# Optimization experiments

Hardware: AMD Instinct MI355X
Metric: run time of the kernel (lower is better)

## Reference

```python
import jax, jax.numpy as jnp
import numpy as np

B, C, H, W, NH = 8, 256, 32, 32, 4  # batch, channels, height, width, heads


def groupnorm(x, w, b, eps=1e-5):
    # GroupNorm with 1 group: normalize over (C,H,W) per sample
    mu = x.mean(axis=(1, 2, 3), keepdims=True)
    var = x.var(axis=(1, 2, 3), keepdims=True)
    xn = (x - mu) * jax.lax.rsqrt(var + eps)
    return xn * w[None, :, None, None] + b[None, :, None, None]


def setup_inputs() -> dict:
    key = jax.random.key(0)
    ks = jax.random.split(key, 6)
    C4 = 4 * C
    s = lambda k, shape, scale: jax.random.normal(k, shape, jnp.float32) * scale
    return {
        "x": jax.random.normal(ks[0], (B, C, H, W), jnp.float32),
        "qkv_w": s(ks[1], (3 * C, C), 0.05),   # 1x1 conv, no bias
        "uh_w": s(ks[2], (C, C), 0.05),
        "uh_b": jnp.zeros((C,), jnp.float32),
        "n1_w": jnp.ones((C,), jnp.float32),
        "n1_b": jnp.zeros((C,), jnp.float32),
        "n2_w": jnp.ones((C,), jnp.float32),
        "n2_b": jnp.zeros((C,), jnp.float32),
        "f1_w": s(ks[3], (C4, C), 0.05),
        "f1_b": jnp.zeros((C4,), jnp.float32),
        "f2_w": s(ks[4], (C, C4), 0.05),
        "f2_b": jnp.zeros((C,), jnp.float32),
        # torch inits these to 0; use nonzero values so both branches contribute
        "gamma_attn": jnp.array(0.5, jnp.float32),
        "gamma_ffn": jnp.array(0.5, jnp.float32),
    }


def reference(x, qkv_w, uh_w, uh_b, n1_w, n1_b, n2_w, n2_b,
              f1_w, f1_b, f2_w, f2_b, gamma_attn, gamma_ffn):
    Bx, Cx, Hx, Wx = x.shape
    N = Hx * Wx
    dk = Cx // NH
    # --- attention branch (eval mode: DropPath is identity) ---
    xn = groupnorm(x, n1_w, n1_b).reshape(Bx, Cx, N)
    qkv = jnp.einsum('oc,bcn->bon', qkv_w, xn)          # 1x1 conv == channel matmul
    q, k, v = [t.reshape(Bx, NH, dk, N) for t in jnp.split(qkv, 3, axis=1)]
    scores = jnp.einsum('bhdi,bhdj->bhij', q, k) / np.float32(np.sqrt(dk))
    attn = jax.nn.softmax(scores, axis=-1)               # [B,H,N,N]
    out = jnp.einsum('bhij,bhdj->bhdi', attn, v).reshape(Bx, Cx, N)
    uh = jnp.einsum('oc,bcn->bon', uh_w, out) + uh_b[None, :, None]
    x2 = x + gamma_attn * uh.reshape(Bx, Cx, Hx, Wx)
    # --- FFN branch ---
    h = groupnorm(x2, n2_w, n2_b).reshape(Bx, Cx, N)
    h = jax.nn.silu(jnp.einsum('oc,bcn->bon', f1_w, h) + f1_b[None, :, None])
    h = jnp.einsum('oc,bcn->bon', f2_w, h) + f2_b[None, :, None]
    return x2 + gamma_ffn * h.reshape(Bx, Cx, Hx, Wx)
```

## Files before the change

kernel.cpp:

```cpp
#include <hip/hip_runtime.h>
#include <math.h>

#define Bsz 8
#define Cch 256
#define Nsp 1024
#define NHd 4
#define QS  0.18033688011112042f

using bf16x8  = __attribute__((ext_vector_type(8))) short;
using f32x4   = __attribute__((ext_vector_type(4))) float;
using ushort8 = __attribute__((ext_vector_type(8))) unsigned short;
#define MFMA(a,b,c) __builtin_amdgcn_mfma_f32_16x16x32_bf16(a,b,c,0,0,0)

__device__ inline unsigned short f2bf(float f) {
    unsigned int u = __float_as_uint(f);
    u = u + 0x7fffu + ((u >> 16) & 1u);
    return (unsigned short)(u >> 16);
}
__device__ inline float bf2f(unsigned short u) {
    return __uint_as_float((unsigned int)u << 16);
}
__device__ inline unsigned int cvtpk(float lo, float hi) {
    unsigned int r;
    asm("v_cvt_pk_bf16_f32 %0, %1, %2" : "=v"(r) : "v"(lo), "v"(hi));
    return r;
}

__global__ __launch_bounds__(256) void wconv_gn(const float* __restrict__ a, const float* __restrict__ b,
                                                const float* __restrict__ c, const float* __restrict__ d,
                                                unsigned short* __restrict__ o,
                                                const float* __restrict__ x,
                                                float* __restrict__ part) {
    if (blockIdx.x < 3072) {
        size_t i = (size_t)blockIdx.x * 256 + threadIdx.x;
        float v;
        if (i < 196608) v = a[i];
        else if (i < 262144) v = b[i - 196608];
        else if (i < 524288) v = c[i - 262144];
        else v = d[i - 524288];
        o[i] = f2bf(v);
        return;
    }
    int blk = blockIdx.x - 3072;
    int bb = blk >> 6;
    const float* xb = x + (size_t)bb * (Cch * Nsp) + (size_t)(blk & 63) * 4096;
    int t = threadIdx.x;
    float s = 0.f, s2 = 0.f;
    for (int i = t; i < 4096; i += 256) { float v = xb[i]; s += v; s2 += v * v; }
    __shared__ float sh[256], sh2[256];
    sh[t] = s; sh2[t] = s2; __syncthreads();
    for (int off = 128; off; off >>= 1) {
        if (t < off) { sh[t] += sh[t + off]; sh2[t] += sh2[t + off]; }
        __syncthreads();
    }
    if (t == 0) { part[blk * 2] = sh[0]; part[blk * 2 + 1] = sh2[0]; }
}

template<int K, int KL, int NFRAG>
__global__ __launch_bounds__(256, 4) void gemm_lds(
        const unsigned short* __restrict__ W,
        const unsigned short* __restrict__ Xcl,
        int epi, int act, int xmode,
        unsigned short* __restrict__ ocl, int Ocl, int ocol0,
        unsigned short* __restrict__ orm,
        float* __restrict__ pf, const float* __restrict__ res,
        unsigned short* __restrict__ x2cl,
        const float* __restrict__ gamma, const float* __restrict__ bias,
        float* __restrict__ part,
        const float* __restrict__ gnpart,
        const float* __restrict__ gnw, const float* __restrict__ gnb) {
    static_assert(KL == 256, "K-loop hardcoded for KL=256 (8 steps)");
    constexpr int NTILE = NFRAG * 16;
    constexpr int CPR = KL / 8;
    constexpr int TOTCH = NTILE * CPR;
    int z = blockIdx.z, nb = blockIdx.x, ob = blockIdx.y;
    int b = (epi == 4) ? (z & 7) : z;
    int kofs = (epi == 4) ? (z >> 3) * KL : 0;
    int t = threadIdx.x, w = t >> 6, l = t & 63, lg = l >> 4, lm = l & 15;
    __shared__ unsigned short Xs[NTILE * KL];
    __shared__ float sgn[2];
    const unsigned short* Xb = Xcl + ((size_t)b * Nsp + nb * NTILE) * K + kofs;
    int o_base = ob * 256 + w * 64;
    const unsigned short* Wp = W + (size_t)(o_base + lm) * K + kofs + 8 * lg;
    int m8 = lm & 7;

    bf16x8 wA0, wA1, wA2, wA3, wB0, wB1, wB2, wB3, wC0, wC1, wC2, wC3;
    #define WL(d0, d1, d2, d3, ks_) do {                                   \
        d0 = *(const bf16x8*)(Wp + (size_t)(0)      + (ks_) * 32);         \
        d1 = *(const bf16x8*)(Wp + (size_t)16 * K   + (ks_) * 32);         \
        d2 = *(const bf16x8*)(Wp + (size_t)32 * K   + (ks_) * 32);         \
        d3 = *(const bf16x8*)(Wp + (size_t)48 * K   + (ks_) * 32);         \
    } while (0)
    WL(wA0, wA1, wA2, wA3, 0);
    WL(wB0, wB1, wB2, wB3, 1);

    if (xmode == 0) {
        #pragma unroll
        for (int i = 0; i < TOTCH / 256; i++) {
            int c = i * 256 + t;
            int n = c / CPR, s = c % CPR;
            int gc = s ^ (n & 7);
            *(bf16x8*)&Xs[c * 8] = *(const bf16x8*)(Xb + (size_t)n * K + gc * 8);
        }
    } else if (xmode == 1) {
        if (t < 64) {
            float s = gnpart[(b * 64 + t) * 2], s2 = gnpart[(b * 64 + t) * 2 + 1];
            for (int m = 1; m < 64; m <<= 1) { s += __shfl_xor(s, m); s2 += __shfl_xor(s2, m); }
            if (t == 0) {
                float inv_n = 1.f / (Cch * Nsp);
                float mu = s * inv_n;
                float var = s2 * inv_n - mu * mu;
                sgn[0] = mu; sgn[1] = rsqrtf(var + 1e-5f);
            }
        }
        __syncthreads();
        float mu = sgn[0], rs = sgn[1];
        #pragma unroll
        for (int i = 0; i < TOTCH / 256; i++) {
            int c = i * 256 + t;
            int n = c / CPR, s = c % CPR;
            int gc = s ^ (n & 7);
            ushort8 xv = *(const ushort8*)(Xb + (size_t)n * K + gc * 8);
            f32x4 w0 = *(const f32x4*)(gnw + gc * 8);
            f32x4 w1 = *(const f32x4*)(gnw + gc * 8 + 4);
            f32x4 b0 = *(const f32x4*)(gnb + gc * 8);
            f32x4 b1 = *(const f32x4*)(gnb + gc * 8 + 4);
            ushort8 rr;
            #pragma unroll
            for (int j = 0; j < 4; j++) {
                rr[j]     = f2bf((bf2f(xv[j])     - mu) * rs * w0[j] + b0[j]);
                rr[4 + j] = f2bf((bf2f(xv[4 + j]) - mu) * rs * w1[j] + b1[j]);
            }
            *(ushort8*)&Xs[c * 8] = rr;
        }
    } else if (xmode == 2) {
        const size_t SPO = (size_t)Bsz * Nsp * Cch;
        #pragma unroll
        for (int i = 0; i < TOTCH / 256; i++) {
            int c = i * 256 + t;
            int n = c / CPR, s = c % CPR;
            int gc = s ^ (n & 7);
            const unsigned short* p0 = Xb + (size_t)n * K + gc * 8;
            int h = gc >> 3;
            int gn = nb * NTILE + n;
            float a0[8] = {};
            float lsum = 0.f;
            #pragma unroll
            for (int sp = 0; sp < 4; sp++) {
                ushort8 ov = *(const ushort8*)(p0 + (size_t)sp * SPO);
                #pragma unroll
                for (int j = 0; j < 8; j++) a0[j] += bf2f(ov[j]);
                lsum += gnpart[(((size_t)sp * Bsz + b) * NHd + h) * Nsp + gn];
            }
            float inv = 1.f / lsum;
            ushort8 rr;
            #pragma unroll
            for (int j = 0; j < 8; j++) rr[j] = f2bf(a0[j] * inv);
            *(ushort8*)&Xs[c * 8] = rr;
        }
    } else {
        if (t < 64) {
            float s = gnpart[(b * 64 + t) * 2], s2 = gnpart[(b * 64 + t) * 2 + 1];
            for (int m = 1; m < 64; m <<= 1) { s += __shfl_xor(s, m); s2 += __shfl_xor(s2, m); }
            if (t == 0) {
                float inv_n = 1.f / (Cch * Nsp);
                float mu = s * inv_n;
                float var = s2 * inv_n - mu * mu;
                sgn[0] = mu; sgn[1] = rsqrtf(var + 1e-5f);
            }
        }
        __syncthreads();
        float mu = sgn[0], rs = sgn[1];
        int n = t & 31;
        #pragma unroll
        for (int i = 0; i < 4; i++) {
            int G = i * 8 + (t >> 5);
            const float* xr = res + ((size_t)b * Cch + G * 8) * Nsp + (size_t)nb * NTILE + n;
            ushort8 rr;
            #pragma unroll
            for (int j = 0; j < 8; j++) {
                float val = xr[(size_t)j * Nsp];
                rr[j] = f2bf((val - mu) * rs * gnw[G * 8 + j] + gnb[G * 8 + j]);
            }
            int slot = G ^ (n & 7);
            *(ushort8*)&Xs[(n * 32 + slot) * 8] = rr;
        }
    }
    __syncthreads();

    f32x4 acc[4][NFRAG] = {};
    #define KS(w0_, w1_, w2_, w3_, ks_) do {                               \
        _Pragma("unroll")                                                  \
        for (int nf = 0; nf < NFRAG; nf++) {                               \
            int slot = ((ks_) * 4 + lg) ^ m8;                              \
            bf16x8 xf = *(const bf16x8*)&Xs[((nf * 16 + lm) * CPR + slot) * 8]; \
            acc[0][nf] = MFMA(w0_, xf, acc[0][nf]);                        \
            acc[1][nf] = MFMA(w1_, xf, acc[1][nf]);                        \
            acc[2][nf] = MFMA(w2_, xf, acc[2][nf]);                        \
            acc[3][nf] = MFMA(w3_, xf, acc[3][nf]);                        \
        }                                                                  \
    } while (0)
    WL(wC0, wC1, wC2, wC3, 2); KS(wA0, wA1, wA2, wA3, 0);
    WL(wA0, wA1, wA2, wA3, 3); KS(wB0, wB1, wB2, wB3, 1);
    WL(wB0, wB1, wB2, wB3, 4); KS(wC0, wC1, wC2, wC3, 2);
    WL(wC0, wC1, wC2, wC3, 5); KS(wA0, wA1, wA2, wA3, 3);
    WL(wA0, wA1, wA2, wA3, 6); KS(wB0, wB1, wB2, wB3, 4);
    WL(wB0, wB1, wB2, wB3, 7); KS(wC0, wC1, wC2, wC3, 5);
    KS(wA0, wA1, wA2, wA3, 6);
    KS(wB0, wB1, wB2, wB3, 7);
    #undef WL
    #undef KS

    if (epi == 0) {
        if (act == 3 && o_base >= 512) {
            #pragma unroll
            for (int nf = 0; nf < NFRAG; nf++) {
                int n = nb * NTILE + nf * 16 + lm;
                #pragma unroll
                for (int q = 0; q < 4; q++)
                    #pragma unroll
                    for (int r = 0; r < 4; r++) {
                        int o = o_base + q * 16 + 4 * lg + r - 512;
                        orm[((size_t)b * Cch + o) * Nsp + n] = f2bf(acc[q][nf][r]);
                    }
            }
        } else {
            float sc = (act == 3 && o_base < 256) ? QS : 1.f;
            #pragma unroll
            for (int nf = 0; nf < NFRAG; nf++) {
                int n = nb * NTILE + nf * 16 + lm;
                unsigned short* dst = ocl + ((size_t)b * Nsp + n) * Ocl + ocol0 + o_base + 4 * lg;
                #pragma unroll
                for (int q = 0; q < 4; q++) {
                    unsigned long long pk = 0;
                    #pragma unroll
                    for (int r = 0; r < 4; r++) {
                        int o = o_base + q * 16 + 4 * lg + r;
                        float v = acc[q][nf][r];
                        if (bias) v += bias[o];
                        if (act == 1) v = v / (1.f + __expf(-v));
                        else v *= sc;
                        pk |= (unsigned long long)f2bf(v) << (16 * r);
                    }
                    *(unsigned long long*)(dst + q * 16) = pk;
                }
            }
        }
    } else if (epi == 2) {
        float g = gamma[0];
        float ps = 0.f, ps2 = 0.f;
        #pragma unroll
        for (int nf = 0; nf < NFRAG; nf++) {
            int n = nb * NTILE + nf * 16 + lm;
            unsigned short* cdst = x2cl + ((size_t)b * Nsp + n) * Cch + o_base + 4 * lg;
            #pragma unroll
            for (int q = 0; q < 4; q++) {
                unsigned long long pk = 0;
                #pragma unroll
                for (int r = 0; r < 4; r++) {
                    int o = o_base + q * 16 + 4 * lg + r;
                    float v = acc[q][nf][r];
                    if (bias) v += bias[o];
                    size_t idx = ((size_t)b * Cch + o) * Nsp + n;
                    float ov = res[idx] + g * v;
                    pf[idx] = ov;
                    ps += ov; ps2 += ov * ov;
                    pk |= (unsigned long long)f2bf(ov) << (16 * r);
                }
                *(unsigned long long*)(cdst + q * 16) = pk;
            }
        }
        float* rsh  = (float*)&Xs[0];
        float* rsh2 = rsh + 256;
        __syncthreads();
        rsh[t] = ps; rsh2[t] = ps2; __syncthreads();
        for (int off = 128; off; off >>= 1) {
            if (t < off) { rsh[t] += rsh[t + off]; rsh2[t] += rsh2[t + off]; }
            __syncthreads();
        }
        if (t == 0) {
            int slot = b * gridDim.x + nb;
            part[slot * 2] = rsh[0]; part[slot * 2 + 1] = rsh2[0];
        }
    } else {
        #pragma unroll
        for (int nf = 0; nf < NFRAG; nf++) {
            int n = nb * NTILE + nf * 16 + lm;
            #pragma unroll
            for (int q = 0; q < 4; q++) {
                unsigned long long pk = 0;
                #pragma unroll
                for (int r = 0; r < 4; r++)
                    pk |= (unsigned long long)f2bf(acc[q][nf][r]) << (16 * r);
                unsigned short* dst = &orm[((size_t)z * Cch + o_base + q * 16 + 4 * lg) * Nsp + n];
                dst[0] = (unsigned short)(pk);
                dst[Nsp] = (unsigned short)(pk >> 16);
                dst[2 * Nsp] = (unsigned short)(pk >> 32);
                dst[3 * Nsp] = (unsigned short)(pk >> 48);
            }
        }
    }
}

__global__ __launch_bounds__(256) void f2_fin(const unsigned short* __restrict__ p,
                                              const float* __restrict__ x2,
                                              const float* __restrict__ bias,
                                              const float* __restrict__ gamma,
                                              float* __restrict__ out) {
    int idx = blockIdx.x * 256 + threadIdx.x;
    size_t e = (size_t)idx * 8;
    int o = (int)((e >> 10) & 255);
    const size_t SPO = (size_t)Bsz * Cch * Nsp;
    float acc[8] = {};
    #pragma unroll
    for (int sp = 0; sp < 4; sp++) {
        ushort8 v = *(const ushort8*)(p + sp * SPO + e);
        #pragma unroll
        for (int j = 0; j < 8; j++) acc[j] += bf2f(v[j]);
    }
    float g = gamma[0], bo = bias[o];
    f32x4 x0 = *(const f32x4*)(x2 + e);
    f32x4 x1 = *(const f32x4*)(x2 + e + 4);
    f32x4 r0, r1;
    #pragma unroll
    for (int j = 0; j < 4; j++) {
        r0[j] = x0[j] + g * (acc[j] + bo);
        r1[j] = x1[j] + g * (acc[4 + j] + bo);
    }
    *(f32x4*)(out + e) = r0;
    *(f32x4*)(out + e + 4) = r1;
}

__global__ __launch_bounds__(256) void attn_mfma8(const unsigned short* __restrict__ qk,
                                                  const unsigned short* __restrict__ v,
                                                  unsigned short* __restrict__ Opart,
                                                  float* __restrict__ lpart) {
    int L = blockIdx.x;
    int xcd = L & 7, jj = L >> 3;
    int g = xcd * 4 + (jj >> 5);
    int m = jj & 31;
    int h = g & 3, b = g >> 2;
    int ib = m & 7, sp = m >> 3;
    int t = threadIdx.x, w = t >> 6, l = t & 63, lg = l >> 4, lm = l & 15;
    __shared__ unsigned short KVs[2][4096];
    __shared__ unsigned short P[4][2][32][36];
    int i0 = ib * 128 + w * 32;
    int j0 = sp * 256;
    const unsigned short* qb = qk + ((size_t)b * Nsp + i0 + lm) * 512 + h * 64 + 8 * lg;
    bf16x8 qf00 = *(const bf16x8*)(qb);
    bf16x8 qf01 = *(const bf16x8*)(qb + 32);
    bf16x8 qf10 = *(const bf16x8*)(qb + 16 * 512);
    bf16x8 qf11 = *(const bf16x8*)(qb + 16 * 512 + 32);

    const unsigned short *gs0, *gs1;
    int lo0, lo1;
    size_t gstep;
    if (t < 128) {
        int c = 2 * t;
        int r = c >> 3, s = c & 7, swr = r & 7;
        const unsigned short* rowp = qk + ((size_t)b * Nsp + j0 + r) * 512 + 256 + h * 64;
        gs0 = rowp + ((s ^ swr) * 8);
        gs1 = rowp + (((s + 1) ^ swr) * 8);
        lo0 = c * 8; lo1 = lo0 + 8;
        gstep = (size_t)32 * 512;
    } else {
        int c = 2 * (t - 128);
        int d = c >> 2, s = c & 3, swd = d & 3;
        const unsigned short* rowp = v + ((size_t)b * Cch + h * 64 + d) * Nsp + j0;
        gs0 = rowp + ((s ^ swd) * 8);
        gs1 = rowp + (((s + 1) ^ swd) * 8);
        lo0 = 2048 + c * 8; lo1 = lo0 + 8;
        gstep = 32;
    }
    int cA = (lg ^ (lm & 7)) * 8;
    int cB = ((4 + lg) ^ (lm & 7)) * 8;
    int cV = (lg ^ (lm & 3)) * 8;

    f32x4 O00 = {}, O01 = {}, O02 = {}, O03 = {};
    f32x4 O10 = {}, O11 = {}, O12 = {}, O13 = {};
    float ls0 = 0.f, ls1 = 0.f;
    bf16x8 sg0, sg1;

    #define ISSUE(tile) do { sg0 = *(const bf16x8*)(gs0 + (size_t)(tile) * gstep); \
                             sg1 = *(const bf16x8*)(gs1 + (size_t)(tile) * gstep); } while (0)
    #define WRITE(bu) do { *(bf16x8*)&KVs[bu][lo0] = sg0; \
                           *(bf16x8*)&KVs[bu][lo1] = sg1; } while (0)
    #define QKC8(bu, pb) do {                                                     \
        const unsigned short* Ka = KVs[bu] + lm * 64;                             \
        const unsigned short* Kc = KVs[bu] + (16 + lm) * 64;                      \
        bf16x8 k00 = *(const bf16x8*)(Ka + cA);                                   \
        bf16x8 k01 = *(const bf16x8*)(Ka + cB);                                   \
        bf16x8 k10 = *(const bf16x8*)(Kc + cA);                                   \
        bf16x8 k11 = *(const bf16x8*)(Kc + cB);                                   \
        f32x4 s00 = {}, s01 = {}, s10 = {}, s11 = {};                             \
        s00 = MFMA(k00, qf00, s00); s00 = MFMA(k01, qf01, s00);                   \
        s01 = MFMA(k00, qf10, s01); s01 = MFMA(k01, qf11, s01);                   \
        s10 = MFMA(k10, qf00, s10); s10 = MFMA(k11, qf01, s10);                   \
        s11 = MFMA(k10, qf10, s11); s11 = MFMA(k11, qf11, s11);                   \
        float p0, p1, p2, p3; uint2 pk;                                           \
        p0 = exp2f(s00[0]); p1 = exp2f(s00[1]); p2 = exp2f(s00[2]); p3 = exp2f(s00[3]); \
        ls0 += (p0 + p1) + (p2 + p3);                                             \
        pk.x = cvtpk(p0, p1); pk.y = cvtpk(p2, p3);                               \
        *(uint2*)&P[w][pb][lm][4 * lg] = pk;                                      \
        p0 = exp2f(s01[0]); p1 = exp2f(s01[1]); p2 = exp2f(s01[2]); p3 = exp2f(s01[3]); \
        ls1 += (p0 + p1) + (p2 + p3);                                             \
        pk.x = cvtpk(p0, p1); pk.y = cvtpk(p2, p3);                               \
        *(uint2*)&P[w][pb][16 + lm][4 * lg] = pk;                                 \
        p0 = exp2f(s10[0]); p1 = exp2f(s10[1]); p2 = exp2f(s10[2]); p3 = exp2f(s10[3]); \
        ls0 += (p0 + p1) + (p2 + p3);                                             \
        pk.x = cvtpk(p0, p1); pk.y = cvtpk(p2, p3);                               \
        *(uint2*)&P[w][pb][lm][16 + 4 * lg] = pk;                                 \
        p0 = exp2f(s11[0]); p1 = exp2f(s11[1]); p2 = exp2f(s11[2]); p3 = exp2f(s11[3]); \
        ls1 += (p0 + p1) + (p2 + p3);                                             \
        pk.x = cvtpk(p0, p1); pk.y = cvtpk(p2, p3);                               \
        *(uint2*)&P[w][pb][16 + lm][16 + 4 * lg] = pk;                            \
    } while (0)
    #define PVC8(bu, pb) do {                                                     \
        bf16x8 pa0 = *(const bf16x8*)&P[w][pb][lm][8 * lg];                       \
        bf16x8 pa1 = *(const bf16x8*)&P[w][pb][16 + lm][8 * lg];                  \
        const unsigned short* Vl = KVs[bu] + 2048;                                \
        bf16x8 v0 = *(const bf16x8*)(Vl + lm * 32 + cV);                          \
        bf16x8 v1 = *(const bf16x8*)(Vl + (16 + lm) * 32 + cV);                   \
        bf16x8 v2 = *(const bf16x8*)(Vl + (32 + lm) * 32 + cV);                   \
        bf16x8 v3 = *(const bf16x8*)(Vl + (48 + lm) * 32 + cV);                   \
        O00 = MFMA(v0, pa0, O00); O10 = MFMA(v0, pa1, O10);                       \
        O01 = MFMA(v1, pa0, O01); O11 = MFMA(v1, pa1, O11);                       \
        O02 = MFMA(v2, pa0, O02); O12 = MFMA(v2, pa1, O12);                       \
        O03 = MFMA(v3, pa0, O03); O13 = MFMA(v3, pa1, O13);                       \
    } while (0)

    ISSUE(0); WRITE(0); __syncthreads();
    ISSUE(1);
    QKC8(0, 0);
    __syncthreads();
    WRITE(1);
    __syncthreads();
    #pragma unroll
    for (int tt = 1; tt < 8; tt++) {
        if (tt < 7) ISSUE(tt + 1);
        QKC8(tt & 1, tt & 1);
        PVC8((tt - 1) & 1, (tt - 1) & 1);
        __syncthreads();
        if (tt < 7) WRITE((tt + 1) & 1);
        __syncthreads();
    }
    PVC8(1, 1);
    #undef ISSUE
    #undef WRITE
    #undef QKC8
    #undef PVC8

    ls0 += __shfl_xor(ls0, 16); ls0 += __shfl_xor(ls0, 32);
    ls1 += __shfl_xor(ls1, 16); ls1 += __shfl_xor(ls1, 32);
    if (lg == 0) {
        float* lp = lpart + (((size_t)sp * Bsz + b) * NHd + h) * Nsp + i0 + lm;
        lp[0] = ls0;
        lp[16] = ls1;
    }
    unsigned short* ob0 = Opart + (((size_t)sp * Bsz + b) * Nsp + i0 + lm) * Cch + h * 64 + 4 * lg;
    unsigned short* ob1 = ob0 + (size_t)16 * Cch;
    uint2 pk;
    #define STO(dt, Oa, Ob_) \
        pk.x = cvtpk(Oa[0], Oa[1]); pk.y = cvtpk(Oa[2], Oa[3]); \
        *(uint2*)(ob0 + dt * 16) = pk; \
        pk.x = cvtpk(Ob_[0], Ob_[1]); pk.y = cvtpk(Ob_[2], Ob_[3]); \
        *(uint2*)(ob1 + dt * 16) = pk;
    STO(0, O00, O10) STO(1, O01, O11) STO(2, O02, O12) STO(3, O03, O13)
    #undef STO
}

extern "C" void kernel_launch(void* const* d_in, const int* in_sizes, int n_in,
                              void* d_out, int out_size, void* d_ws, size_t ws_size,
                              hipStream_t stream) {
    const float* x      = (const float*)d_in[0];
    const float* qkv_w  = (const float*)d_in[1];
    const float* uh_w   = (const float*)d_in[2];
    const float* uh_b   = (const float*)d_in[3];
    const float* n1_w   = (const float*)d_in[4];
    const float* n1_b   = (const float*)d_in[5];
    const float* n2_w   = (const float*)d_in[6];
    const float* n2_b   = (const float*)d_in[7];
    const float* f1_w   = (const float*)d_in[8];
    const float* f1_b   = (const float*)d_in[9];
    const float* f2_w   = (const float*)d_in[10];
    const float* f2_b   = (const float*)d_in[11];
    const float* g_attn = (const float*)d_in[12];
    const float* g_ffn  = (const float*)d_in[13];
    float* out = (float*)d_out;
    char* ws = (char*)d_ws;

    float*          part1   = (float*)(ws + 1024);
    float*          part2   = (float*)(ws + 5120);
    unsigned short* wbf     = (unsigned short*)(ws + 16384);
    float*          lpart   = (float*)(ws + 2097152);
    unsigned short* qk_cl   = (unsigned short*)(ws + 6291456);
    unsigned short* vbuf    = (unsigned short*)(ws + 14680064);
    unsigned short* x2cl    = (unsigned short*)(ws + 14680064);
    unsigned short* Opart   = (unsigned short*)(ws + 23068672);
    float*          x2      = (float*)(ws + 50331648);
    unsigned short* praw_bf = (unsigned short*)(ws + 67108864);
    unsigned short* h1_cl   = (unsigned short*)(ws + 100663296);

    unsigned short* wbf_qkv = wbf;
    unsigned short* wbf_uh  = wbf + 196608;
    unsigned short* wbf_f1  = wbf + 262144;
    unsigned short* wbf_f2  = wbf + 524288;

    wconv_gn<<<3584, 256, 0, stream>>>(qkv_w, uh_w, f1_w, f2_w, wbf, x, part1);

    gemm_lds<256, 256, 2><<<dim3(32, 3, Bsz), 256, 0, stream>>>(wbf_qkv,
        (const unsigned short*)x, 0, 3, 3,
        qk_cl, 512, 0, vbuf, nullptr, x, nullptr, nullptr, nullptr, nullptr,
        part1, n1_w, n1_b);
    attn_mfma8<<<1024, 256, 0, stream>>>(qk_cl, vbuf, Opart, lpart);
    gemm_lds<256, 256, 1><<<dim3(64, 1, Bsz), 256, 0, stream>>>(wbf_uh, Opart, 2, 0, 2,
        nullptr, 0, 0, nullptr, x2, x, x2cl, g_attn, uh_b, part2,
        lpart, nullptr, nullptr);

    gemm_lds<256, 256, 2><<<dim3(32, 4, Bsz), 256, 0, stream>>>(wbf_f1, x2cl, 0, 1, 1,
        h1_cl, 1024, 0, nullptr, nullptr, nullptr, nullptr, nullptr, f1_b, nullptr,
        part2, n2_w, n2_b);
    gemm_lds<1024, 256, 2><<<dim3(32, 1, 32), 256, 0, stream>>>(wbf_f2, h1_cl, 4, 0, 0,
        nullptr, 0, 0, praw_bf, nullptr, nullptr, nullptr, nullptr, nullptr, nullptr,
        nullptr, nullptr, nullptr);
    f2_fin<<<1024, 256, 0, stream>>>(praw_bf, x2, f2_b, g_ffn, out);
}
```

Before: 121.2 us.

## Replace split-K f2 GEMM plus reduction with single full-K fused kernel

Removes the split-K path for the second FFN matmul, which wrote four bf16 partial outputs and needed a separate reduction kernel. Adds a dedicated kernel that runs the full K=1024 loop per block with double-buffered LDS staging and register-rotated weight loads, then applies bias, gamma and the residual add directly in its epilogue. This drops the partial-buffer round trip and one launch. In exchange each block does four times the K work, with a smaller 64-output tile over 32 positions, and the output stores are narrower.

```diff
diff --git a/kernel.cpp b/kernel.cpp
--- a/kernel.cpp
+++ b/kernel.cpp
@@ -69,19 +69,17 @@
         float* __restrict__ part,
         const float* __restrict__ gnpart,
         const float* __restrict__ gnw, const float* __restrict__ gnb) {
-    static_assert(KL == 256, "K-loop hardcoded for KL=256 (8 steps)");
+    static_assert(KL == 256 && K == 256, "single-round K only");
     constexpr int NTILE = NFRAG * 16;
     constexpr int CPR = KL / 8;
     constexpr int TOTCH = NTILE * CPR;
-    int z = blockIdx.z, nb = blockIdx.x, ob = blockIdx.y;
-    int b = (epi == 4) ? (z & 7) : z;
-    int kofs = (epi == 4) ? (z >> 3) * KL : 0;
+    int b = blockIdx.z, nb = blockIdx.x, ob = blockIdx.y;
     int t = threadIdx.x, w = t >> 6, l = t & 63, lg = l >> 4, lm = l & 15;
     __shared__ unsigned short Xs[NTILE * KL];
     __shared__ float sgn[2];
-    const unsigned short* Xb = Xcl + ((size_t)b * Nsp + nb * NTILE) * K + kofs;
+    const unsigned short* Xb = Xcl + ((size_t)b * Nsp + nb * NTILE) * K;
     int o_base = ob * 256 + w * 64;
-    const unsigned short* Wp = W + (size_t)(o_base + lm) * K + kofs + 8 * lg;
+    const unsigned short* Wp = W + (size_t)(o_base + lm) * K + 8 * lg;
     int m8 = lm & 7;
 
     bf16x8 wA0, wA1, wA2, wA3, wB0, wB1, wB2, wB3, wC0, wC1, wC2, wC3;
@@ -246,7 +244,7 @@
                 }
             }
         }
-    } else if (epi == 2) {
+    } else {
         float g = gamma[0];
         float ps = 0.f, ps2 = 0.f;
         #pragma unroll
@@ -282,53 +280,120 @@
             int slot = b * gridDim.x + nb;
             part[slot * 2] = rsh[0]; part[slot * 2 + 1] = rsh2[0];
         }
-    } else {
-        #pragma unroll
-        for (int nf = 0; nf < NFRAG; nf++) {
-            int n = nb * NTILE + nf * 16 + lm;
-            #pragma unroll
-            for (int q = 0; q < 4; q++) {
-                unsigned long long pk = 0;
-                #pragma unroll
-                for (int r = 0; r < 4; r++)
-                    pk |= (unsigned long long)f2bf(acc[q][nf][r]) << (16 * r);
-                unsigned short* dst = &orm[((size_t)z * Cch + o_base + q * 16 + 4 * lg) * Nsp + n];
-                dst[0] = (unsigned short)(pk);
-                dst[Nsp] = (unsigned short)(pk >> 16);
-                dst[2 * Nsp] = (unsigned short)(pk >> 32);
-                dst[3 * Nsp] = (unsigned short)(pk >> 48);
-            }
-        }
-    }
-}
-
-__global__ __launch_bounds__(256) void f2_fin(const unsigned short* __restrict__ p,
-                                              const float* __restrict__ x2,
-                                              const float* __restrict__ bias,
-                                              const float* __restrict__ gamma,
-                                              float* __restrict__ out) {
-    int idx = blockIdx.x * 256 + threadIdx.x;
-    size_t e = (size_t)idx * 8;
-    int o = (int)((e >> 10) & 255);
-    const size_t SPO = (size_t)Bsz * Cch * Nsp;
-    float acc[8] = {};
+    }
+}
+
+__global__ __launch_bounds__(256, 4) void f2k(
+        const unsigned short* __restrict__ Wf2,
+        const unsigned short* __restrict__ h1,
+        const float* __restrict__ f2b,
+        const float* __restrict__ gamma,
+        const float* __restrict__ x2,
+        float* __restrict__ out) {
+    int b = blockIdx.z, nb = blockIdx.x, ob = blockIdx.y;
+    int t = threadIdx.x, w = t >> 6, l = t & 63, lg = l >> 4, lm = l & 15;
+    __shared__ unsigned short Xs0[32 * 256];
+    __shared__ unsigned short Xs1[32 * 256];
+    const unsigned short* Xb = h1 + ((size_t)b * Nsp + nb * 32) * 1024;
+    int m8 = lm & 7;
+    const unsigned short* Wp2 = Wf2 + (size_t)(ob * 64 + w * 16 + lm) * 1024 + 8 * lg;
+
+    bf16x8 ua, ub, uc, ud, ue, uf;
+    #define WL2(d0, ks_) d0 = *(const bf16x8*)(Wp2 + (ks_) * 32)
+    WL2(ua, 0); WL2(ub, 1); WL2(uc, 2); WL2(ud, 3);
+
+    int c0 = t, c1 = 256 + t, c2 = 512 + t, c3 = 768 + t;
+    int n0 = c0 >> 5, n1 = c1 >> 5, n2 = c2 >> 5, n3 = c3 >> 5;
+    const unsigned short* p0 = Xb + (size_t)n0 * 1024 + ((c0 & 31) ^ (n0 & 7)) * 8;
+    const unsigned short* p1 = Xb + (size_t)n1 * 1024 + ((c1 & 31) ^ (n1 & 7)) * 8;
+    const unsigned short* p2 = Xb + (size_t)n2 * 1024 + ((c2 & 31) ^ (n2 & 7)) * 8;
+    const unsigned short* p3 = Xb + (size_t)n3 * 1024 + ((c3 & 31) ^ (n3 & 7)) * 8;
+
+    *(bf16x8*)&Xs0[c0 * 8] = *(const bf16x8*)(p0);
+    *(bf16x8*)&Xs1[c0 * 8] = *(const bf16x8*)(p0 + 256);
+    *(bf16x8*)&Xs0[c1 * 8] = *(const bf16x8*)(p1);
+    *(bf16x8*)&Xs1[c1 * 8] = *(const bf16x8*)(p1 + 256);
+    *(bf16x8*)&Xs0[c2 * 8] = *(const bf16x8*)(p2);
+    *(bf16x8*)&Xs1[c2 * 8] = *(const bf16x8*)(p2 + 256);
+    *(bf16x8*)&Xs0[c3 * 8] = *(const bf16x8*)(p3);
+    *(bf16x8*)&Xs1[c3 * 8] = *(const bf16x8*)(p3 + 256);
+    __syncthreads();
+
+    f32x4 ac0 = {}, ac1 = {};
+    bf16x8 st0, st1, st2, st3;
+    #define FISSUE(r_) do {                                     \
+        st0 = *(const bf16x8*)(p0 + (r_) * 256);                \
+        st1 = *(const bf16x8*)(p1 + (r_) * 256);                \
+        st2 = *(const bf16x8*)(p2 + (r_) * 256);                \
+        st3 = *(const bf16x8*)(p3 + (r_) * 256);                \
+    } while (0)
+    #define FWRITE(Bf) do {                                     \
+        *(bf16x8*)&Bf[c0 * 8] = st0;                            \
+        *(bf16x8*)&Bf[c1 * 8] = st1;                            \
+        *(bf16x8*)&Bf[c2 * 8] = st2;                            \
+        *(bf16x8*)&Bf[c3 * 8] = st3;                            \
+    } while (0)
+    #define KS2(e0, ks_, Xp) do {                               \
+        int slot = ((ks_) * 4 + lg) ^ m8;                       \
+        bf16x8 xf0 = *(const bf16x8*)&Xp[((lm) * 32 + slot) * 8];        \
+        ac0 = MFMA(e0, xf0, ac0);                               \
+        bf16x8 xf1 = *(const bf16x8*)&Xp[((16 + lm) * 32 + slot) * 8];   \
+        ac1 = MFMA(e0, xf1, ac1);                               \
+    } while (0)
+
+    WL2(ue, 4);  KS2(ua, 0, Xs0);
+    WL2(uf, 5);  KS2(ub, 1, Xs0);
+    WL2(ua, 6);  KS2(uc, 2, Xs0);
+    WL2(ub, 7);  KS2(ud, 3, Xs0);
+    FISSUE(2);
+    WL2(uc, 8);  KS2(ue, 4, Xs0);
+    WL2(ud, 9);  KS2(uf, 5, Xs0);
+    WL2(ue, 10); KS2(ua, 6, Xs0);
+    WL2(uf, 11); KS2(ub, 7, Xs0);
+    __syncthreads();
+    FWRITE(Xs0);
+    WL2(ua, 12); KS2(uc, 0, Xs1);
+    WL2(ub, 13); KS2(ud, 1, Xs1);
+    WL2(uc, 14); KS2(ue, 2, Xs1);
+    WL2(ud, 15); KS2(uf, 3, Xs1);
+    FISSUE(3);
+    WL2(ue, 16); KS2(ua, 4, Xs1);
+    WL2(uf, 17); KS2(ub, 5, Xs1);
+    WL2(ua, 18); KS2(uc, 6, Xs1);
+    WL2(ub, 19); KS2(ud, 7, Xs1);
+    __syncthreads();
+    FWRITE(Xs1);
+    WL2(uc, 20); KS2(ue, 0, Xs0);
+    WL2(ud, 21); KS2(uf, 1, Xs0);
+    WL2(ue, 22); KS2(ua, 2, Xs0);
+    WL2(uf, 23); KS2(ub, 3, Xs0);
+    WL2(ua, 24); KS2(uc, 4, Xs0);
+    WL2(ub, 25); KS2(ud, 5, Xs0);
+    WL2(uc, 26); KS2(ue, 6, Xs0);
+    WL2(ud, 27); KS2(uf, 7, Xs0);
+    __syncthreads();
+    WL2(ue, 28); KS2(ua, 0, Xs1);
+    WL2(uf, 29); KS2(ub, 1, Xs1);
+    WL2(ua, 30); KS2(uc, 2, Xs1);
+    WL2(ub, 31); KS2(ud, 3, Xs1);
+    KS2(ue, 4, Xs1);
+    KS2(uf, 5, Xs1);
+    KS2(ua, 6, Xs1);
+    KS2(ub, 7, Xs1);
+    #undef WL2
+    #undef KS2
+    #undef FISSUE
+    #undef FWRITE
+
+    float gm = gamma[0];
     #pragma unroll
-    for (int sp = 0; sp < 4; sp++) {
-        ushort8 v = *(const ushort8*)(p + sp * SPO + e);
-        #pragma unroll
-        for (int j = 0; j < 8; j++) acc[j] += bf2f(v[j]);
-    }
-    float g = gamma[0], bo = bias[o];
-    f32x4 x0 = *(const f32x4*)(x2 + e);
-    f32x4 x1 = *(const f32x4*)(x2 + e + 4);
-    f32x4 r0, r1;
-    #pragma unroll
-    for (int j = 0; j < 4; j++) {
-        r0[j] = x0[j] + g * (acc[j] + bo);
-        r1[j] = x1[j] + g * (acc[4 + j] + bo);
-    }
-    *(f32x4*)(out + e) = r0;
-    *(f32x4*)(out + e + 4) = r1;
+    for (int rr = 0; rr < 4; rr++) {
+        int o = ob * 64 + w * 16 + 4 * lg + rr;
+        float bo = f2b[o];
+        size_t row = ((size_t)b * Cch + o) * Nsp + nb * 32;
+        out[row + lm]      = x2[row + lm]      + gm * (ac0[rr] + bo);
+        out[row + 16 + lm] = x2[row + 16 + lm] + gm * (ac1[rr] + bo);
+    }
 }
 
 __global__ __launch_bounds__(256) void attn_mfma8(const unsigned short* __restrict__ qk,
@@ -498,8 +563,7 @@
     unsigned short* x2cl    = (unsigned short*)(ws + 14680064);
     unsigned short* Opart   = (unsigned short*)(ws + 23068672);
     float*          x2      = (float*)(ws + 50331648);
-    unsigned short* praw_bf = (unsigned short*)(ws + 67108864);
-    unsigned short* h1_cl   = (unsigned short*)(ws + 100663296);
+    unsigned short* h1_cl   = (unsigned short*)(ws + 67108864);
 
     unsigned short* wbf_qkv = wbf;
     unsigned short* wbf_uh  = wbf + 196608;
@@ -520,8 +584,5 @@
     gemm_lds<256, 256, 2><<<dim3(32, 4, Bsz), 256, 0, stream>>>(wbf_f1, x2cl, 0, 1, 1,
         h1_cl, 1024, 0, nullptr, nullptr, nullptr, nullptr, nullptr, f1_b, nullptr,
         part2, n2_w, n2_b);
-    gemm_lds<1024, 256, 2><<<dim3(32, 1, 32), 256, 0, stream>>>(wbf_f2, h1_cl, 4, 0, 0,
-        nullptr, 0, 0, praw_bf, nullptr, nullptr, nullptr, nullptr, nullptr, nullptr,
-        nullptr, nullptr, nullptr);
-    f2_fin<<<1024, 256, 0, stream>>>(praw_bf, x2, f2_b, g_ffn, out);
-}
+    f2k<<<dim3(32, 4, Bsz), 256, 0, stream>>>(wbf_f2, h1_cl, f2_b, g_ffn, x2, out);
+}
```

After: 116.1 us. 4.2% less time.
